# Kernel optimization log

Hardware: AMD Instinct MI355X
Metric: run time of the kernel (lower is better)

The kernel has to match this reference:

```python
import jax, jax.numpy as jnp
import numpy as np

B, T, C = 2, 2048, 2048
H, KVH = 16, 4
HD = C // H            # head_dim = 128
REP = H // KVH         # q heads per kv head = 4


def _alibi_slopes(n_head):
    # get_slopes_power_of_2: start = 2^(-2^-(log2(H)-3)); s_h = start * start^h
    start = 2.0 ** (-(2.0 ** (-(np.log2(n_head) - 3.0))))
    return jnp.asarray([start ** (i + 1) for i in range(n_head)], jnp.float32)


def setup_inputs() -> dict:
    key = jax.random.key(0)
    ks = jax.random.split(key, 4)
    sc = 0.02
    return {
        "x": jax.random.normal(ks[0], (B, T, C), jnp.float32),
        "Wq": jax.random.normal(ks[1], (C, C), jnp.float32) * sc,
        "Wkv": jax.random.normal(ks[2], (C, HD * KVH * 2), jnp.float32) * sc,
        "Wo": jax.random.normal(ks[3], (C, C), jnp.float32) * sc,
        "bo": jnp.zeros((C,), jnp.float32),
    }


def reference(x, Wq, Wkv, Wo, bo):
    Bv, Tv, Cv = x.shape
    # projections
    q = (x @ Wq).reshape(Bv, Tv, H, HD).transpose(0, 2, 1, 3)      # (B,H,T,hd)
    k, v = jnp.split(x @ Wkv, 2, axis=-1)
    k = k.reshape(Bv, Tv, KVH, HD).transpose(0, 2, 1, 3)           # (B,KVH,T,hd)
    v = v.reshape(Bv, Tv, KVH, HD).transpose(0, 2, 1, 3)
    # torch .repeat tiles kv heads: query head h = r*KVH + g uses kv head g.
    qg = q.reshape(Bv, REP, KVH, Tv, HD)
    scores = jnp.einsum('brgtd,bgsd->brgts', qg, k) / jnp.sqrt(jnp.float32(HD))
    # ALiBi bias: tril((j - i) * slope_h), zero on/above diagonal region handled by causal mask
    idx = jnp.arange(Tv)
    diff = (idx[None, :] - idx[:, None]).astype(jnp.float32)       # j - i (negative below diag)
    slopes = _alibi_slopes(H).reshape(REP, KVH)                    # head h = r*KVH+g
    bias = jnp.tril(diff)[None, None] * slopes[:, :, None, None]   # (REP,KVH,T,T)
    causal = idx[None, :] <= idx[:, None]                          # (T,T)
    scores = jnp.where(causal[None, None, None], scores + bias[None], -jnp.inf)
    attn = jax.nn.softmax(scores, axis=-1)
    out = jnp.einsum('brgts,bgsd->brgtd', attn, v)                 # (B,REP,KVH,T,hd)
    out = out.reshape(Bv, H, Tv, HD).transpose(0, 2, 1, 3).reshape(Bv, Tv, Cv)
    return out @ Wo + bo
```

## Files before the change

kernel.cpp:

```cpp
#include <hip/hip_runtime.h>

typedef __attribute__((ext_vector_type(8))) __bf16 bf16x8;
typedef __attribute__((ext_vector_type(4))) float f32x4;

#define NEG_BIG (-1e30f)

__device__ __forceinline__ unsigned short f2b(float f) {
    unsigned int u = __float_as_uint(f);
    u += 0x7FFFu + ((u >> 16) & 1u);
    return (unsigned short)(u >> 16);
}
__device__ __forceinline__ float b2f(unsigned short h) {
    return __uint_as_float(((unsigned int)h) << 16);
}
__device__ __forceinline__ unsigned cvtpk(float lo, float hi) {
    unsigned r;
    asm("v_cvt_pk_bf16_f32 %0, %1, %2" : "=v"(r) : "v"(lo), "v"(hi));
    return r;
}

typedef const __attribute__((address_space(1))) unsigned int* gas_ptr;
typedef __attribute__((address_space(3))) unsigned int* las_ptr;
__device__ __forceinline__ void gload16(const void* g, void* l) {
    __builtin_amdgcn_global_load_lds((gas_ptr)g, (las_ptr)l, 16, 0, 0);
}

__global__ __launch_bounds__(256) void k_convert(
    const float* __restrict__ x, unsigned short* __restrict__ xb, int n4)
{
    int i = blockIdx.x * 256 + threadIdx.x;
    if (i >= n4) return;
    float4 v = reinterpret_cast<const float4*>(x)[i];
    ushort4 h;
    h.x = f2b(v.x); h.y = f2b(v.y); h.z = f2b(v.z); h.w = f2b(v.w);
    reinterpret_cast<ushort4*>(xb)[i] = h;
}

__global__ __launch_bounds__(256) void k_transpose(
    const float* __restrict__ W, unsigned short* __restrict__ Th, int K, int N)
{
    __shared__ float tile[64][65];
    const int n0 = blockIdx.x * 64, k0 = blockIdx.y * 64;
    const int c = threadIdx.x & 63, r0 = threadIdx.x >> 6;
    for (int rr = r0; rr < 64; rr += 4)
        tile[rr][c] = W[(size_t)(k0 + rr) * N + n0 + c];
    __syncthreads();
    for (int rr = r0; rr < 64; rr += 4)
        Th[(size_t)(n0 + rr) * K + k0 + c] = f2b(tile[c][rr]);
}

__global__ __launch_bounds__(256) void k_gemm(
    const unsigned short* __restrict__ A, const unsigned short* __restrict__ B,
    void* __restrict__ CoutA, int NA, void* __restrict__ CoutB, int NB, int N1,
    const float* __restrict__ bias, int M, int K, int outF32)
{
    __shared__ __align__(16) unsigned short As[128][64];
    __shared__ __align__(16) unsigned short Bs[128][64];

    const int tid  = threadIdx.x;
    const int lane = tid & 63, wid = tid >> 6;
    const int wr = wid >> 1, wc = wid & 1;
    const int lrow = lane & 15, lko = (lane >> 4) << 3;
    const int bm = blockIdx.y, bn = blockIdx.x;

    const int srow = tid >> 3;
    const int scol = ((tid & 7) ^ (srow & 7)) << 3;
    const int wbase = wid * 1024;

    const int sw = (lrow & 7) << 3;
    const int c0 = lko ^ sw;
    const int c1 = (32 + lko) ^ sw;

    f32x4 acc[4][4] = {};

    const size_t aoff = (size_t)(bm * 128 + srow) * K + scol;
    const size_t boff = (size_t)(bn * 128 + srow) * K + scol;
    const size_t slab = (size_t)32 * K;

    for (int k0 = 0; k0 < K; k0 += 64) {
        #pragma unroll
        for (int s = 0; s < 4; ++s) {
            gload16(&A[aoff + s * slab + k0], (char*)&As[0][0] + s * 4096 + wbase);
            gload16(&B[boff + s * slab + k0], (char*)&Bs[0][0] + s * 4096 + wbase);
        }
        __syncthreads();

        #pragma unroll
        for (int kk2 = 0; kk2 < 2; ++kk2) {
            const int cc = kk2 ? c1 : c0;
            bf16x8 af[4], bf[4];
            #pragma unroll
            for (int m = 0; m < 4; ++m)
                af[m] = *reinterpret_cast<const bf16x8*>(&As[wr * 64 + m * 16 + lrow][cc]);
            #pragma unroll
            for (int n = 0; n < 4; ++n)
                bf[n] = *reinterpret_cast<const bf16x8*>(&Bs[wc * 64 + n * 16 + lrow][cc]);
            #pragma unroll
            for (int m = 0; m < 4; ++m)
                #pragma unroll
                for (int n = 0; n < 4; ++n)
                    acc[m][n] = __builtin_amdgcn_mfma_f32_16x16x32_bf16(af[m], bf[n], acc[m][n], 0, 0, 0);
        }
        __syncthreads();
    }

    const int rbase = bm * 128 + wr * 64 + ((lane >> 4) << 2);
    const int cbase = bn * 128 + wc * 64 + lrow;
    #pragma unroll
    for (int m = 0; m < 4; ++m)
        #pragma unroll
        for (int n = 0; n < 4; ++n) {
            const int col = cbase + n * 16;
            const float bv = bias ? bias[col] : 0.0f;
            const bool inA = (col < N1);
            const int ccol = inA ? col : (col - N1);
            const int cstr = inA ? NA : NB;
            void* base = inA ? CoutA : CoutB;
            #pragma unroll
            for (int r = 0; r < 4; ++r) {
                const size_t idx = (size_t)(rbase + m * 16 + r) * cstr + ccol;
                const float v = acc[m][n][r] + bv;
                if (outF32) ((float*)base)[idx] = v;
                else        ((unsigned short*)base)[idx] = f2b(v);
            }
        }
}

__global__ __launch_bounds__(512, 4) void k_attn(
    const unsigned short* __restrict__ Qb,
    const unsigned short* __restrict__ KVb,
    unsigned short* __restrict__ AO)
{
    __shared__ __align__(16) unsigned short Ksl[64][128];
    __shared__ __align__(16) unsigned short Vt[128][72];
    __shared__ __align__(16) unsigned short Psl[8][16][72];

    const int blk = blockIdx.x;
    const int idx = blk >> 3;
    const int sub = blk & 7;
    const int b   = sub >> 2;
    const int g   = sub & 3;
    const int chunk = (idx < 32) ? (63 - idx) : (idx - 32);
    const int q0  = chunk * 32;

    const int tid = threadIdx.x;
    const int lane = tid & 63;
    const int w = tid >> 6;
    const int h = (w & 3) * 4 + g;
    const int q0w = q0 + (w >> 2) * 16;
    const float slope = exp2f(-0.5f * (float)(h + 1));
    const float isq = 0.088388347648318447f;
    const int lrow = lane & 15;
    const int lko  = (lane >> 4) << 3;
    const int rowg = (lane >> 4) << 2;
    const int skey = tid >> 4;
    const int sd0  = (tid & 15) << 3;
    const int vdim = tid & 127;
    const int vkg  = tid >> 7;

    uint4 kreg[2];
    unsigned short vv[2][8];

    auto ldK = [&](int kb) {
        const int j0 = kb << 6;
        #pragma unroll
        for (int pp = 0; pp < 2; ++pp) {
            const int key = skey + pp * 32;
            kreg[pp] = *reinterpret_cast<const uint4*>(
                &KVb[(size_t)(b * 2048 + j0 + key) * 1024 + g * 128 + sd0]);
        }
    };
    auto wrK = [&]() {
        #pragma unroll
        for (int pp = 0; pp < 2; ++pp) {
            const int key = skey + pp * 32;
            *reinterpret_cast<uint4*>(&Ksl[key][sd0 ^ ((key & 7) << 3)]) = kreg[pp];
        }
    };
    auto ldV = [&](int kb) {
        const int j0 = kb << 6;
        #pragma unroll
        for (int gi = 0; gi < 2; ++gi) {
            const int kgi = gi * 4 + vkg;
            const size_t base = (size_t)(b * 2048 + j0 + kgi * 8) * 1024 + 512 + g * 128 + vdim;
            #pragma unroll
            for (int j = 0; j < 8; ++j)
                vv[gi][j] = KVb[base + (size_t)j * 1024];
        }
    };
    auto wrV = [&]() {
        #pragma unroll
        for (int gi = 0; gi < 2; ++gi) {
            const int kgi = gi * 4 + vkg;
            *reinterpret_cast<uint4*>(&Vt[vdim][kgi * 8]) =
                *reinterpret_cast<const uint4*>(&vv[gi][0]);
        }
    };

    bf16x8 qf[4];
    {
        const size_t qoff = (size_t)(b * 2048 + q0w + lrow) * 2048 + h * 128 + lko;
        #pragma unroll
        for (int kk = 0; kk < 4; ++kk)
            qf[kk] = *reinterpret_cast<const bf16x8*>(&Qb[qoff + kk * 32]);
    }

    f32x4 oacc[8] = {};
    float mrow = NEG_BIG, lsum = 0.f;
    const int nkb = (q0 + 32 + 63) >> 6;
    const int q = q0w + lrow;

    ldK(0); ldV(0);
    wrK(); wrV();
    __syncthreads();

    for (int kb = 0; kb < nkb; ++kb) {
        const int j0 = kb << 6;
        const bool pre = (kb + 1 < nkb);
        if (pre) { ldK(kb + 1); ldV(kb + 1); }

        f32x4 sa[4] = {};
        #pragma unroll
        for (int c = 0; c < 4; ++c) {
            const int krow = c * 16 + lrow;
            #pragma unroll
            for (int kk = 0; kk < 4; ++kk) {
                bf16x8 kf = *reinterpret_cast<const bf16x8*>(
                    &Ksl[krow][(kk * 32 + lko) ^ ((krow & 7) << 3)]);
                sa[c] = __builtin_amdgcn_mfma_f32_16x16x32_bf16(kf, qf[kk], sa[c], 0, 0, 0);
            }
        }

        float pv[4][4];
        float mt = NEG_BIG;
        #pragma unroll
        for (int c = 0; c < 4; ++c)
            #pragma unroll
            for (int r = 0; r < 4; ++r) {
                const int j = j0 + c * 16 + rowg + r;
                const float vsc = (j <= q) ? (sa[c][r] * isq + slope * (float)(j - q)) : NEG_BIG;
                pv[c][r] = vsc;
                mt = fmaxf(mt, vsc);
            }
        mt = fmaxf(mt, __shfl_xor(mt, 16));
        mt = fmaxf(mt, __shfl_xor(mt, 32));
        const float mn = fmaxf(mrow, mt);
        const float alpha = __expf(mrow - mn);
        mrow = mn;
        float s = 0.f;
        #pragma unroll
        for (int c = 0; c < 4; ++c)
            #pragma unroll
            for (int r = 0; r < 4; ++r) {
                const float pe = __expf(pv[c][r] - mn);
                pv[c][r] = pe;
                s += pe;
            }
        s += __shfl_xor(s, 16);
        s += __shfl_xor(s, 32);
        lsum = lsum * alpha + s;

        float ar[4];
        #pragma unroll
        for (int r = 0; r < 4; ++r) ar[r] = __shfl(alpha, rowg + r);
        #pragma unroll
        for (int f = 0; f < 8; ++f)
            #pragma unroll
            for (int r = 0; r < 4; ++r)
                oacc[f][r] *= ar[r];

        #pragma unroll
        for (int c = 0; c < 4; ++c) {
            uint2 pw;
            pw.x = cvtpk(pv[c][0], pv[c][1]);
            pw.y = cvtpk(pv[c][2], pv[c][3]);
            *reinterpret_cast<uint2*>(&Psl[w][lrow][c * 16 + rowg]) = pw;
        }
        asm volatile("s_waitcnt lgkmcnt(0)" ::: "memory");

        #pragma unroll
        for (int kk2 = 0; kk2 < 2; ++kk2) {
            bf16x8 pf = *reinterpret_cast<const bf16x8*>(&Psl[w][lrow][kk2 * 32 + lko]);
            #pragma unroll
            for (int nb = 0; nb < 8; ++nb) {
                bf16x8 vf = *reinterpret_cast<const bf16x8*>(&Vt[nb * 16 + lrow][kk2 * 32 + lko]);
                oacc[nb] = __builtin_amdgcn_mfma_f32_16x16x32_bf16(pf, vf, oacc[nb], 0, 0, 0);
            }
        }

        __syncthreads();
        if (pre) { wrK(); wrV(); }
        __syncthreads();
    }

    float lr[4];
    #pragma unroll
    for (int r = 0; r < 4; ++r) lr[r] = __shfl(lsum, rowg + r);
    #pragma unroll
    for (int nb = 0; nb < 8; ++nb)
        #pragma unroll
        for (int r = 0; r < 4; ++r) {
            const int row = q0w + rowg + r;
            const int col = h * 128 + nb * 16 + lrow;
            const float vo = oacc[nb][r] / lr[r];
            AO[(size_t)(b * 2048 + row) * 2048 + col] = f2b(vo);
        }
}

extern "C" void kernel_launch(void* const* d_in, const int* in_sizes, int n_in,
                              void* d_out, int out_size, void* d_ws, size_t ws_size,
                              hipStream_t stream)
{
    const float* x   = (const float*)d_in[0];
    const float* Wq  = (const float*)d_in[1];
    const float* Wkv = (const float*)d_in[2];
    const float* Wo  = (const float*)d_in[3];
    const float* bo  = (const float*)d_in[4];

    char* ws = (char*)d_ws;
    unsigned short* xb  = (unsigned short*)(ws + (size_t)0);
    unsigned short* Wt  = (unsigned short*)(ws + ((size_t)16 << 20));
    unsigned short* Qb  = (unsigned short*)(ws + ((size_t)28 << 20));
    unsigned short* KVb = (unsigned short*)(ws + ((size_t)44 << 20));

    k_convert<<<8192, 256, 0, stream>>>(x, xb, (2 * 2048 * 2048) / 4);

    k_transpose<<<dim3(32, 32), 256, 0, stream>>>(Wq, Wt, 2048, 2048);
    k_transpose<<<dim3(16, 32), 256, 0, stream>>>(Wkv, Wt + (size_t)2048 * 2048, 2048, 1024);

    k_gemm<<<dim3(24, 32), 256, 0, stream>>>(xb, Wt, Qb, 2048, KVb, 1024, 2048,
                                             nullptr, 4096, 2048, 0);

    k_attn<<<512, 512, 0, stream>>>(Qb, KVb, xb);

    k_transpose<<<dim3(32, 32), 256, 0, stream>>>(Wo, Wt, 2048, 2048);
    k_gemm<<<dim3(16, 32), 256, 0, stream>>>(xb, Wt, d_out, 2048, nullptr, 2048, 2048,
                                             bo, 4096, 2048, 1);
}
```

Baseline: 246.7 us.

## Switch attention to 32x32x16 MFMA with register-shuffled P and 4-wave blocks

Rewrites the attention kernel to use 32x32x16 bf16 MFMA tiles, where each wave handles 32 query rows for one head and blocks shrink from 8 waves to 4. The P matrix is now rearranged into the A-operand layout with cross-half lane shuffles instead of being written to and read back from shared memory, which removes the Psl buffer and its waitcnt. This cuts LDS traffic and MFMA instruction count per tile. In exchange it raises register pressure (16-wide accumulators, 8 Q fragments) and halves the threads per block that share each K/V tile load.

```diff
diff --git a/kernel.cpp b/kernel.cpp
--- a/kernel.cpp
+++ b/kernel.cpp
@@ -2,6 +2,7 @@
 
 typedef __attribute__((ext_vector_type(8))) __bf16 bf16x8;
 typedef __attribute__((ext_vector_type(4))) float f32x4;
+typedef __attribute__((ext_vector_type(16))) float f32x16;
 
 #define NEG_BIG (-1e30f)
 
@@ -9,9 +10,6 @@
     unsigned int u = __float_as_uint(f);
     u += 0x7FFFu + ((u >> 16) & 1u);
     return (unsigned short)(u >> 16);
-}
-__device__ __forceinline__ float b2f(unsigned short h) {
-    return __uint_as_float(((unsigned int)h) << 16);
 }
 __device__ __forceinline__ unsigned cvtpk(float lo, float hi) {
     unsigned r;
@@ -126,14 +124,13 @@
         }
 }
 
-__global__ __launch_bounds__(512, 4) void k_attn(
+__global__ __launch_bounds__(256, 2) void k_attn(
     const unsigned short* __restrict__ Qb,
     const unsigned short* __restrict__ KVb,
     unsigned short* __restrict__ AO)
 {
     __shared__ __align__(16) unsigned short Ksl[64][128];
     __shared__ __align__(16) unsigned short Vt[128][72];
-    __shared__ __align__(16) unsigned short Psl[8][16][72];
 
     const int blk = blockIdx.x;
     const int idx = blk >> 3;
@@ -146,42 +143,42 @@
     const int tid = threadIdx.x;
     const int lane = tid & 63;
     const int w = tid >> 6;
-    const int h = (w & 3) * 4 + g;
-    const int q0w = q0 + (w >> 2) * 16;
+    const int h = w * 4 + g;
+    const int ql = lane & 31;
+    const int hb = lane >> 5;
     const float slope = exp2f(-0.5f * (float)(h + 1));
     const float isq = 0.088388347648318447f;
-    const int lrow = lane & 15;
-    const int lko  = (lane >> 4) << 3;
-    const int rowg = (lane >> 4) << 2;
+    const int kswz = (ql & 15) << 3;
+
     const int skey = tid >> 4;
     const int sd0  = (tid & 15) << 3;
     const int vdim = tid & 127;
     const int vkg  = tid >> 7;
 
-    uint4 kreg[2];
-    unsigned short vv[2][8];
+    uint4 kreg[4];
+    unsigned short vv[4][8];
 
     auto ldK = [&](int kb) {
         const int j0 = kb << 6;
         #pragma unroll
-        for (int pp = 0; pp < 2; ++pp) {
-            const int key = skey + pp * 32;
-            kreg[pp] = *reinterpret_cast<const uint4*>(
+        for (int p = 0; p < 4; ++p) {
+            const int key = skey + p * 16;
+            kreg[p] = *reinterpret_cast<const uint4*>(
                 &KVb[(size_t)(b * 2048 + j0 + key) * 1024 + g * 128 + sd0]);
         }
     };
     auto wrK = [&]() {
         #pragma unroll
-        for (int pp = 0; pp < 2; ++pp) {
-            const int key = skey + pp * 32;
-            *reinterpret_cast<uint4*>(&Ksl[key][sd0 ^ ((key & 7) << 3)]) = kreg[pp];
+        for (int p = 0; p < 4; ++p) {
+            const int key = skey + p * 16;
+            *reinterpret_cast<uint4*>(&Ksl[key][sd0 ^ ((key & 15) << 3)]) = kreg[p];
         }
     };
     auto ldV = [&](int kb) {
         const int j0 = kb << 6;
         #pragma unroll
-        for (int gi = 0; gi < 2; ++gi) {
-            const int kgi = gi * 4 + vkg;
+        for (int gi = 0; gi < 4; ++gi) {
+            const int kgi = gi * 2 + vkg;
             const size_t base = (size_t)(b * 2048 + j0 + kgi * 8) * 1024 + 512 + g * 128 + vdim;
             #pragma unroll
             for (int j = 0; j < 8; ++j)
@@ -190,25 +187,25 @@
     };
     auto wrV = [&]() {
         #pragma unroll
-        for (int gi = 0; gi < 2; ++gi) {
-            const int kgi = gi * 4 + vkg;
+        for (int gi = 0; gi < 4; ++gi) {
+            const int kgi = gi * 2 + vkg;
             *reinterpret_cast<uint4*>(&Vt[vdim][kgi * 8]) =
                 *reinterpret_cast<const uint4*>(&vv[gi][0]);
         }
     };
 
-    bf16x8 qf[4];
+    bf16x8 qf[8];
     {
-        const size_t qoff = (size_t)(b * 2048 + q0w + lrow) * 2048 + h * 128 + lko;
-        #pragma unroll
-        for (int kk = 0; kk < 4; ++kk)
-            qf[kk] = *reinterpret_cast<const bf16x8*>(&Qb[qoff + kk * 32]);
+        const size_t qoff = (size_t)(b * 2048 + q0 + ql) * 2048 + h * 128 + 8 * hb;
+        #pragma unroll
+        for (int s = 0; s < 8; ++s)
+            qf[s] = *reinterpret_cast<const bf16x8*>(&Qb[qoff + 16 * s]);
     }
 
-    f32x4 oacc[8] = {};
+    f32x16 oacc[4] = {};
     float mrow = NEG_BIG, lsum = 0.f;
     const int nkb = (q0 + 32 + 63) >> 6;
-    const int q = q0w + lrow;
+    const int q = q0 + ql;
 
     ldK(0); ldV(0);
     wrK(); wrV();
@@ -219,91 +216,102 @@
         const bool pre = (kb + 1 < nkb);
         if (pre) { ldK(kb + 1); ldV(kb + 1); }
 
-        f32x4 sa[4] = {};
-        #pragma unroll
-        for (int c = 0; c < 4; ++c) {
-            const int krow = c * 16 + lrow;
-            #pragma unroll
-            for (int kk = 0; kk < 4; ++kk) {
+        f32x16 sa[2] = {};
+        #pragma unroll
+        for (int c = 0; c < 2; ++c) {
+            const int krow = c * 32 + ql;
+            #pragma unroll
+            for (int s = 0; s < 8; ++s) {
                 bf16x8 kf = *reinterpret_cast<const bf16x8*>(
-                    &Ksl[krow][(kk * 32 + lko) ^ ((krow & 7) << 3)]);
-                sa[c] = __builtin_amdgcn_mfma_f32_16x16x32_bf16(kf, qf[kk], sa[c], 0, 0, 0);
-            }
-        }
-
-        float pv[4][4];
+                    &Ksl[krow][(16 * s + 8 * hb) ^ kswz]);
+                sa[c] = __builtin_amdgcn_mfma_f32_32x32x16_bf16(kf, qf[s], sa[c], 0, 0, 0);
+            }
+        }
+
         float mt = NEG_BIG;
         #pragma unroll
-        for (int c = 0; c < 4; ++c)
-            #pragma unroll
-            for (int r = 0; r < 4; ++r) {
-                const int j = j0 + c * 16 + rowg + r;
-                const float vsc = (j <= q) ? (sa[c][r] * isq + slope * (float)(j - q)) : NEG_BIG;
-                pv[c][r] = vsc;
-                mt = fmaxf(mt, vsc);
-            }
-        mt = fmaxf(mt, __shfl_xor(mt, 16));
+        for (int c = 0; c < 2; ++c)
+            #pragma unroll
+            for (int r = 0; r < 16; ++r) {
+                const int j = j0 + 32 * c + (r & 3) + 8 * (r >> 2) + 4 * hb;
+                const float v = (j <= q) ? (sa[c][r] * isq + slope * (float)(j - q)) : NEG_BIG;
+                sa[c][r] = v;
+                mt = fmaxf(mt, v);
+            }
         mt = fmaxf(mt, __shfl_xor(mt, 32));
         const float mn = fmaxf(mrow, mt);
         const float alpha = __expf(mrow - mn);
         mrow = mn;
-        float s = 0.f;
-        #pragma unroll
-        for (int c = 0; c < 4; ++c)
-            #pragma unroll
-            for (int r = 0; r < 4; ++r) {
-                const float pe = __expf(pv[c][r] - mn);
-                pv[c][r] = pe;
-                s += pe;
-            }
-        s += __shfl_xor(s, 16);
-        s += __shfl_xor(s, 32);
-        lsum = lsum * alpha + s;
-
-        float ar[4];
-        #pragma unroll
-        for (int r = 0; r < 4; ++r) ar[r] = __shfl(alpha, rowg + r);
-        #pragma unroll
-        for (int f = 0; f < 8; ++f)
-            #pragma unroll
-            for (int r = 0; r < 4; ++r)
-                oacc[f][r] *= ar[r];
-
-        #pragma unroll
-        for (int c = 0; c < 4; ++c) {
-            uint2 pw;
-            pw.x = cvtpk(pv[c][0], pv[c][1]);
-            pw.y = cvtpk(pv[c][2], pv[c][3]);
-            *reinterpret_cast<uint2*>(&Psl[w][lrow][c * 16 + rowg]) = pw;
-        }
-        asm volatile("s_waitcnt lgkmcnt(0)" ::: "memory");
-
-        #pragma unroll
-        for (int kk2 = 0; kk2 < 2; ++kk2) {
-            bf16x8 pf = *reinterpret_cast<const bf16x8*>(&Psl[w][lrow][kk2 * 32 + lko]);
-            #pragma unroll
-            for (int nb = 0; nb < 8; ++nb) {
-                bf16x8 vf = *reinterpret_cast<const bf16x8*>(&Vt[nb * 16 + lrow][kk2 * 32 + lko]);
-                oacc[nb] = __builtin_amdgcn_mfma_f32_16x16x32_bf16(pf, vf, oacc[nb], 0, 0, 0);
-            }
-        }
+        float ssum = 0.f;
+        #pragma unroll
+        for (int c = 0; c < 2; ++c)
+            #pragma unroll
+            for (int r = 0; r < 16; ++r) {
+                const float pe = __expf(sa[c][r] - mn);
+                sa[c][r] = pe;
+                ssum += pe;
+            }
+        ssum += __shfl_xor(ssum, 32);
+        lsum = lsum * alpha + ssum;
+
+        float ar[16];
+        #pragma unroll
+        for (int r = 0; r < 16; ++r)
+            ar[r] = __shfl(alpha, (r & 3) + 8 * (r >> 2) + 4 * hb);
+        #pragma unroll
+        for (int nb = 0; nb < 4; ++nb)
+            #pragma unroll
+            for (int r = 0; r < 16; ++r)
+                oacc[nb][r] *= ar[r];
+
+        unsigned pw[2][8];
+        #pragma unroll
+        for (int c = 0; c < 2; ++c)
+            #pragma unroll
+            for (int i = 0; i < 8; ++i)
+                pw[c][i] = cvtpk(sa[c][2 * i], sa[c][2 * i + 1]);
+
+        bf16x8 pA[4];
+        #pragma unroll
+        for (int s4 = 0; s4 < 4; ++s4) {
+            const int half = s4 >> 1, a = 4 * (s4 & 1);
+            const unsigned xw0 = hb ? pw[half][a]     : pw[half][a + 2];
+            const unsigned xw1 = hb ? pw[half][a + 1] : pw[half][a + 3];
+            const unsigned rx0 = (unsigned)__shfl_xor((int)xw0, 32);
+            const unsigned rx1 = (unsigned)__shfl_xor((int)xw1, 32);
+            union { unsigned u[4]; bf16x8 v; } f;
+            f.u[0] = hb ? rx0 : pw[half][a];
+            f.u[1] = hb ? rx1 : pw[half][a + 1];
+            f.u[2] = hb ? pw[half][a + 2] : rx0;
+            f.u[3] = hb ? pw[half][a + 3] : rx1;
+            pA[s4] = f.v;
+        }
+
+        #pragma unroll
+        for (int s4 = 0; s4 < 4; ++s4)
+            #pragma unroll
+            for (int nb = 0; nb < 4; ++nb) {
+                bf16x8 vf = *reinterpret_cast<const bf16x8*>(
+                    &Vt[nb * 32 + ql][16 * s4 + 8 * hb]);
+                oacc[nb] = __builtin_amdgcn_mfma_f32_32x32x16_bf16(pA[s4], vf, oacc[nb], 0, 0, 0);
+            }
 
         __syncthreads();
         if (pre) { wrK(); wrV(); }
         __syncthreads();
     }
 
-    float lr[4];
+    float lr[16];
     #pragma unroll
-    for (int r = 0; r < 4; ++r) lr[r] = __shfl(lsum, rowg + r);
+    for (int r = 0; r < 16; ++r)
+        lr[r] = __shfl(lsum, (r & 3) + 8 * (r >> 2) + 4 * hb);
     #pragma unroll
-    for (int nb = 0; nb < 8; ++nb)
-        #pragma unroll
-        for (int r = 0; r < 4; ++r) {
-            const int row = q0w + rowg + r;
-            const int col = h * 128 + nb * 16 + lrow;
-            const float vo = oacc[nb][r] / lr[r];
-            AO[(size_t)(b * 2048 + row) * 2048 + col] = f2b(vo);
+    for (int nb = 0; nb < 4; ++nb)
+        #pragma unroll
+        for (int r = 0; r < 16; ++r) {
+            const int row = q0 + (r & 3) + 8 * (r >> 2) + 4 * hb;
+            const int col = h * 128 + nb * 32 + ql;
+            AO[(size_t)(b * 2048 + row) * 2048 + col] = f2b(oacc[nb][r] / lr[r]);
         }
 }
 
@@ -331,7 +339,7 @@
     k_gemm<<<dim3(24, 32), 256, 0, stream>>>(xb, Wt, Qb, 2048, KVb, 1024, 2048,
                                              nullptr, 4096, 2048, 0);
 
-    k_attn<<<512, 512, 0, stream>>>(Qb, KVb, xb);
+    k_attn<<<512, 256, 0, stream>>>(Qb, KVb, xb);
 
     k_transpose<<<dim3(32, 32), 256, 0, stream>>>(Wo, Wt, 2048, 2048);
     k_gemm<<<dim3(16, 32), 256, 0, stream>>>(xb, Wt, d_out, 2048, nullptr, 2048, 2048,
```

Result: slower. 254.2 us (+3.0%).
